# Optimization experiments

Measured on AMD Instinct MI355X. Metric: run time of the kernel, lower is better.

The kernel has to match this reference:

```python
import jax, jax.numpy as jnp
from jax import lax
import numpy as np

S, B, I, H = 1024, 512, 5, 32
G = 4 * H  # torch LSTM gate dim, order: i, f, g, o


def setup_inputs() -> dict:
    key = jax.random.key(0)
    ks = jax.random.split(key, 19)
    n = lambda k, shape, s=0.1: jax.random.normal(k, shape, jnp.float32) * s
    return {
        "x": jax.random.normal(ks[0], (S, B, I), jnp.float32),
        "Wih0": n(ks[1], (G, I)), "Whh0": n(ks[2], (G, H)), "bih0": n(ks[3], (G,)), "bhh0": n(ks[4], (G,)),
        "Wih1": n(ks[5], (G, H)), "Whh1": n(ks[6], (G, H)), "bih1": n(ks[7], (G,)), "bhh1": n(ks[8], (G,)),
        "Wih2": n(ks[9], (G, H)), "Whh2": n(ks[10], (G, H)), "bih2": n(ks[11], (G,)), "bhh2": n(ks[12], (G,)),
        "w1": n(ks[13], (H, H)), "b1": n(ks[14], (H,)),
        "w2": n(ks[15], (H, H)), "b2": n(ks[16], (H,)),
        "w3": n(ks[17], (1, H)), "b3": n(ks[18], (1,)),
    }


def lstm_layer(x, Wih, Whh, bih, bhh):
    # x: [S, B, in]; precompute input projections for all steps (one big GEMM)
    xp = jnp.einsum("sbi,gi->sbg", x, Wih) + bih + bhh  # [S, B, 4H]
    h0 = jnp.zeros((x.shape[1], H), x.dtype)
    c0 = jnp.zeros((x.shape[1], H), x.dtype)

    def step(carry, xg):
        h, c = carry
        gates = xg + h @ Whh.T  # [B, 4H]
        i, f, g, o = jnp.split(gates, 4, axis=-1)
        c = jax.nn.sigmoid(f) * c + jax.nn.sigmoid(i) * jnp.tanh(g)
        h = jax.nn.sigmoid(o) * jnp.tanh(c)
        return (h, c), h

    _, ys = lax.scan(step, (h0, c0), xp)
    return ys  # [S, B, H]


def reference(x, Wih0, Whh0, bih0, bhh0, Wih1, Whh1, bih1, bhh1,
              Wih2, Whh2, bih2, bhh2, w1, b1, w2, b2, w3, b3):
    h = lstm_layer(x, Wih0, Whh0, bih0, bhh0)
    h = lstm_layer(h, Wih1, Whh1, bih1, bhh1)
    h = lstm_layer(h, Wih2, Whh2, bih2, bhh2)  # [S, B, H]
    s, b, hd = h.shape
    y = h.reshape(s * b, hd)
    y = y @ w1.T + b1
    y = y @ w2.T + b2
    y = y @ w3.T + b3
    y = jax.nn.relu(y)
    return y.reshape(s, b, -1)  # [S, B, 1]
```

## Files before the change

kernel.cpp:

```cpp
#include <hip/hip_runtime.h>
#include <math.h>

#define S_LEN 1024
#define BATCH 512
#define HID   32

#define LOG2E 1.44269504088896340736f

__device__ __forceinline__ float fast_rcp(float x) { return __builtin_amdgcn_rcpf(x); }
__device__ __forceinline__ float fast_exp2(float x) { return __builtin_amdgcn_exp2f(x); }

__device__ __forceinline__ void tick_barrier() {
    asm volatile("s_waitcnt lgkmcnt(0)" ::: "memory");
    __builtin_amdgcn_s_barrier();
    asm volatile("" ::: "memory");
}

typedef unsigned int uint2v __attribute__((ext_vector_type(2)));
__device__ __forceinline__ void swap_halves(float v, float& hiAll, float& loAll) {
    uint2v r = __builtin_amdgcn_permlane32_swap(__float_as_uint(v),
                                                __float_as_uint(v),
                                                false, false);
    hiAll = __uint_as_float(r[0]);
    loAll = __uint_as_float(r[1]);
}

__device__ __forceinline__ float bcast(float v, int k) {
    return __int_as_float(__builtin_amdgcn_readlane(__float_as_int(v), k));
}

__device__ __forceinline__ float wave_sum64_dpp(float v) {
    float s = v;
    s += __int_as_float(__builtin_amdgcn_update_dpp(
             0, __float_as_int(s), 0x111, 0xf, 0xf, true));
    s += __int_as_float(__builtin_amdgcn_update_dpp(
             0, __float_as_int(s), 0x112, 0xf, 0xf, true));
    s += __int_as_float(__builtin_amdgcn_update_dpp(
             0, __float_as_int(s), 0x114, 0xf, 0xf, true));
    s += __int_as_float(__builtin_amdgcn_update_dpp(
             0, __float_as_int(s), 0x118, 0xf, 0xf, true));
    s += __int_as_float(__builtin_amdgcn_update_dpp(
             0, __float_as_int(s), 0x142, 0xa, 0xf, true));
    s += __int_as_float(__builtin_amdgcn_update_dpp(
             0, __float_as_int(s), 0x143, 0xc, 0xf, true));
    return s;
}

#define LOADROW(dst, base, row, sc)                                            \
    {                                                                          \
        const float4* W_ = reinterpret_cast<const float4*>((base) +            \
                                                    (size_t)(row) * HID);      \
        _Pragma("unroll")                                                      \
        for (int k4 = 0; k4 < 8; ++k4) {                                       \
            float4 v_ = W_[k4];                                                \
            dst[4 * k4 + 0] = v_.x * (sc);                                     \
            dst[4 * k4 + 1] = v_.y * (sc);                                     \
            dst[4 * k4 + 2] = v_.z * (sc);                                     \
            dst[4 * k4 + 3] = v_.w * (sc);                                     \
        }                                                                      \
    }

__global__ __launch_bounds__(192)
__attribute__((amdgpu_waves_per_eu(2)))
void lstm3_fused(const float* __restrict__ x,
                 const float* __restrict__ Wih0, const float* __restrict__ Whh0,
                 const float* __restrict__ bih0, const float* __restrict__ bhh0,
                 const float* __restrict__ Wih1, const float* __restrict__ Whh1,
                 const float* __restrict__ bih1, const float* __restrict__ bhh1,
                 const float* __restrict__ Wih2, const float* __restrict__ Whh2,
                 const float* __restrict__ bih2, const float* __restrict__ bhh2,
                 const float* __restrict__ w1, const float* __restrict__ b1,
                 const float* __restrict__ w2, const float* __restrict__ b2,
                 const float* __restrict__ w3, const float* __restrict__ b3,
                 float* __restrict__ out)
{
    const int b = blockIdx.x;
    const int w = threadIdx.x >> 6;
    const int l = threadIdx.x & 63;
    const int j = l & 31;
    const bool lowHalf = (l < 32);
    const int gA = l;
    const int gB = l + 64;
    const float sA = LOG2E;
    const float sB = lowHalf ? (2.0f * LOG2E) : LOG2E;

    __shared__ float4 xl4[S_LEN];
    __shared__ float  xl1[S_LEN];
    __shared__ float ring[4][2][HID];

    for (int i = threadIdx.x; i < 4 * 2 * HID; i += 192)
        (&ring[0][0][0])[i] = 0.0f;
    {
        float* xf = reinterpret_cast<float*>(xl4);
        for (int idx = threadIdx.x; idx < S_LEN * 5; idx += 192) {
            const int s = idx / 5;
            const int c = idx - 5 * s;
            const float v = x[(size_t)s * (BATCH * 5) + b * 5 + c];
            if (c < 4) xf[s * 4 + c] = v;
            else       xl1[s] = v;
        }
    }

    const float* Wih = (w == 0) ? Wih0 : (w == 1) ? Wih1 : Wih2;
    const float* Whh = (w == 0) ? Whh0 : (w == 1) ? Whh1 : Whh2;
    const float* bih = (w == 0) ? bih0 : (w == 1) ? bih1 : bih2;
    const float* bhh = (w == 0) ? bhh0 : (w == 1) ? bhh1 : bhh2;

    float whA[HID], whB[HID];
    LOADROW(whA, Whh, gA, sA);
    LOADROW(whB, Whh, gB, sB);
    float wiA[HID], wiB[HID];
    float wxA[5], wxB[5];
    if (w == 0) {
#pragma unroll
        for (int k = 0; k < 5; ++k) {
            wxA[k] = Wih[gA * 5 + k] * sA;
            wxB[k] = Wih[gB * 5 + k] * sB;
        }
    } else {
        LOADROW(wiA, Wih, gA, sA);
        LOADROW(wiB, Wih, gB, sB);
    }
    const float biasA = (bih[gA] + bhh[gA]) * sA;
    const float biasB = (bih[gB] + bhh[gB]) * sB;

    float v_j = 0.0f, cbias = 0.0f;
    if (w == 2) {
        float uacc[HID];
#pragma unroll
        for (int k = 0; k < HID; ++k) uacc[k] = 0.0f;
        for (int r = 0; r < HID; ++r) {
            const float w3r = w3[r];
#pragma unroll
            for (int k = 0; k < HID; ++k)
                uacc[k] += w3r * w2[r * HID + k];
        }
#pragma unroll
        for (int k = 0; k < HID; ++k) {
            v_j   += uacc[k] * w1[k * HID + j];
            cbias += uacc[k] * b1[k];
        }
        for (int r = 0; r < HID; ++r) cbias += w3[r] * b2[r];
        cbias += b3[0];
        v_j *= 0.5f;
    }

    float c = 0.0f;
    float h_own = 0.0f;

    __syncthreads();

#pragma unroll 1
    for (int t = 0; t < S_LEN + 4; ++t) {
        const int s = t - 2 * w;
        const bool active = (s >= 0) && (s < S_LEN);
        const int wslot = t & 3;
        const int rslot = wslot ^ 2;

        float aA0 = biasA, aA1 = 0.f, aA2 = 0.f, aA3 = 0.f;
        float aB0 = biasB, aB1 = 0.f, aB2 = 0.f, aB3 = 0.f;

#pragma unroll
        for (int k4 = 0; k4 < HID / 4; ++k4) {
            const float h0 = bcast(h_own, 4 * k4 + 0);
            const float h1 = bcast(h_own, 4 * k4 + 1);
            const float h2 = bcast(h_own, 4 * k4 + 2);
            const float h3 = bcast(h_own, 4 * k4 + 3);
            aA0 += whA[4 * k4 + 0] * h0;
            aA1 += whA[4 * k4 + 1] * h1;
            aA2 += whA[4 * k4 + 2] * h2;
            aA3 += whA[4 * k4 + 3] * h3;
            aB0 += whB[4 * k4 + 0] * h0;
            aB1 += whB[4 * k4 + 1] * h1;
            aB2 += whB[4 * k4 + 2] * h2;
            aB3 += whB[4 * k4 + 3] * h3;
        }

        if (w == 0) {
            if (active) {
                const float4 xv = xl4[s];
                const float  x4 = xl1[s];
                aA0 += wxA[0] * xv.x; aB0 += wxB[0] * xv.x;
                aA1 += wxA[1] * xv.y; aB1 += wxB[1] * xv.y;
                aA2 += wxA[2] * xv.z; aB2 += wxB[2] * xv.z;
                aA3 += wxA[3] * xv.w; aB3 += wxB[3] * xv.w;
                aA0 += wxA[4] * x4;   aB0 += wxB[4] * x4;
            }
        } else {
            const float4* hin4 =
                reinterpret_cast<const float4*>(&ring[rslot][w - 1][0]);
#pragma unroll
            for (int k4 = 0; k4 < HID / 4; ++k4) {
                float4 hv = hin4[k4];
                aA0 += wiA[4 * k4 + 0] * hv.x;
                aA1 += wiA[4 * k4 + 1] * hv.y;
                aA2 += wiA[4 * k4 + 2] * hv.z;
                aA3 += wiA[4 * k4 + 3] * hv.w;
                aB0 += wiB[4 * k4 + 0] * hv.x;
                aB1 += wiB[4 * k4 + 1] * hv.y;
                aB2 += wiB[4 * k4 + 2] * hv.z;
                aB3 += wiB[4 * k4 + 3] * hv.w;
            }
        }
        const float accA = (aA0 + aA1) + (aA2 + aA3);
        const float accB = (aB0 + aB1) + (aB2 + aB3);

        float yf, yi, yo, yg;
        swap_halves(accA, yf, yi);
        swap_halves(accB, yo, yg);

        const float gi = fast_rcp(1.0f + fast_exp2(-yi));
        const float gf = fast_rcp(1.0f + fast_exp2(-yf));
        const float sg = fast_rcp(1.0f + fast_exp2(-yg));
        const float go = fast_rcp(1.0f + fast_exp2(-yo));
        const float gg = 2.0f * sg - 1.0f;

        const float c_new = gf * c + gi * gg;
        const float e  = fast_exp2(-2.0f * LOG2E * fabsf(c_new));
        const float tc = copysignf((1.0f - e) * fast_rcp(1.0f + e), c_new);
        const float h = go * tc;

        if (active) {
            c = c_new;
            h_own = h;
            if (w < 2) {
                if (lowHalf) ring[wslot][w][j] = h;
            } else {
                const float tot = wave_sum64_dpp(h * v_j);
                const float y = fmaxf(tot + cbias, 0.0f);
                if (l == 63)
                    out[(size_t)s * BATCH + b] = y;
            }
        }
        if (t & 1) tick_barrier();
    }
}

extern "C" void kernel_launch(void* const* d_in, const int* in_sizes, int n_in,
                              void* d_out, int out_size, void* d_ws, size_t ws_size,
                              hipStream_t stream)
{
    const float* x    = (const float*)d_in[0];
    const float* Wih0 = (const float*)d_in[1];
    const float* Whh0 = (const float*)d_in[2];
    const float* bih0 = (const float*)d_in[3];
    const float* bhh0 = (const float*)d_in[4];
    const float* Wih1 = (const float*)d_in[5];
    const float* Whh1 = (const float*)d_in[6];
    const float* bih1 = (const float*)d_in[7];
    const float* bhh1 = (const float*)d_in[8];
    const float* Wih2 = (const float*)d_in[9];
    const float* Whh2 = (const float*)d_in[10];
    const float* bih2 = (const float*)d_in[11];
    const float* bhh2 = (const float*)d_in[12];
    const float* w1   = (const float*)d_in[13];
    const float* b1   = (const float*)d_in[14];
    const float* w2   = (const float*)d_in[15];
    const float* b2   = (const float*)d_in[16];
    const float* w3   = (const float*)d_in[17];
    const float* b3   = (const float*)d_in[18];

    lstm3_fused<<<BATCH, 192, 0, stream>>>(x, Wih0, Whh0, bih0, bhh0,
                                           Wih1, Whh1, bih1, bhh1,
                                           Wih2, Whh2, bih2, bhh2,
                                           w1, b1, w2, b2, w3, b3,
                                           (float*)d_out);
}
```

Baseline: 848.1 us.

## Run all three LSTM layers sequentially in one wave per batch element

Replaces the three-wave, layer-pipelined block (one wave per layer, communicating through an LDS ring with barriers) with a single 64-thread wave that computes all three layers each timestep. Whh0/Whh1 stay in registers, while Wih1, Wih2 and Whh2 are staged into LDS with an XOR swizzle to avoid bank conflicts. The layer-2 recurrent matvec is issued early to overlap with the layer-0 work. This removes the per-tick block barriers and the ring traffic. In exchange each wave's serial chain per step becomes roughly three times longer, and it relies on LDS reads plus more register pressure.

```diff
diff --git a/kernel.cpp b/kernel.cpp
--- a/kernel.cpp
+++ b/kernel.cpp
@@ -9,12 +9,6 @@
 
 __device__ __forceinline__ float fast_rcp(float x) { return __builtin_amdgcn_rcpf(x); }
 __device__ __forceinline__ float fast_exp2(float x) { return __builtin_amdgcn_exp2f(x); }
-
-__device__ __forceinline__ void tick_barrier() {
-    asm volatile("s_waitcnt lgkmcnt(0)" ::: "memory");
-    __builtin_amdgcn_s_barrier();
-    asm volatile("" ::: "memory");
-}
 
 typedef unsigned int uint2v __attribute__((ext_vector_type(2)));
 __device__ __forceinline__ void swap_halves(float v, float& hiAll, float& loAll) {
@@ -60,72 +54,62 @@
         }                                                                      \
     }
 
-__global__ __launch_bounds__(192)
-__attribute__((amdgpu_waves_per_eu(2)))
-void lstm3_fused(const float* __restrict__ x,
-                 const float* __restrict__ Wih0, const float* __restrict__ Whh0,
-                 const float* __restrict__ bih0, const float* __restrict__ bhh0,
-                 const float* __restrict__ Wih1, const float* __restrict__ Whh1,
-                 const float* __restrict__ bih1, const float* __restrict__ bhh1,
-                 const float* __restrict__ Wih2, const float* __restrict__ Whh2,
-                 const float* __restrict__ bih2, const float* __restrict__ bhh2,
-                 const float* __restrict__ w1, const float* __restrict__ b1,
-                 const float* __restrict__ w2, const float* __restrict__ b2,
-                 const float* __restrict__ w3, const float* __restrict__ b3,
-                 float* __restrict__ out)
+__global__ __launch_bounds__(64, 1)
+void lstm3_seq(const float* __restrict__ x,
+               const float* __restrict__ Wih0, const float* __restrict__ Whh0,
+               const float* __restrict__ bih0, const float* __restrict__ bhh0,
+               const float* __restrict__ Wih1, const float* __restrict__ Whh1,
+               const float* __restrict__ bih1, const float* __restrict__ bhh1,
+               const float* __restrict__ Wih2, const float* __restrict__ Whh2,
+               const float* __restrict__ bih2, const float* __restrict__ bhh2,
+               const float* __restrict__ w1, const float* __restrict__ b1,
+               const float* __restrict__ w2, const float* __restrict__ b2,
+               const float* __restrict__ w3, const float* __restrict__ b3,
+               float* __restrict__ out)
 {
     const int b = blockIdx.x;
-    const int w = threadIdx.x >> 6;
     const int l = threadIdx.x & 63;
     const int j = l & 31;
     const bool lowHalf = (l < 32);
     const int gA = l;
     const int gB = l + 64;
+    const int andA = l & 7;
     const float sA = LOG2E;
     const float sB = lowHalf ? (2.0f * LOG2E) : LOG2E;
 
-    __shared__ float4 xl4[S_LEN];
-    __shared__ float  xl1[S_LEN];
-    __shared__ float ring[4][2][HID];
-
-    for (int i = threadIdx.x; i < 4 * 2 * HID; i += 192)
-        (&ring[0][0][0])[i] = 0.0f;
+    __shared__ float wlds[3 * 128 * 32];
+
+    for (int i4 = l; i4 < 3 * 1024; i4 += 64) {
+        const int set = i4 >> 10;
+        const int rem = i4 & 1023;
+        const int row = rem >> 3;
+        const int k4  = rem & 7;
+        const float* W = (set == 0) ? Wih1 : (set == 1) ? Wih2 : Whh2;
+        float4 v = *reinterpret_cast<const float4*>(W + row * HID + k4 * 4);
+        const float sc = (row >= 64 && row < 96) ? 2.0f * LOG2E : LOG2E;
+        v.x *= sc; v.y *= sc; v.z *= sc; v.w *= sc;
+        *reinterpret_cast<float4*>(
+            &wlds[(set << 12) + row * HID + ((k4 ^ (row & 7)) << 2)]) = v;
+    }
+
+    float whA0[HID], whB0[HID], whA1[HID], whB1[HID];
+    LOADROW(whA0, Whh0, gA, sA); LOADROW(whB0, Whh0, gB, sB);
+    LOADROW(whA1, Whh1, gA, sA); LOADROW(whB1, Whh1, gB, sB);
+    float wxA[5], wxB[5];
+#pragma unroll
+    for (int k = 0; k < 5; ++k) {
+        wxA[k] = Wih0[gA * 5 + k] * sA;
+        wxB[k] = Wih0[gB * 5 + k] * sB;
+    }
+    const float b0A = (bih0[gA] + bhh0[gA]) * sA;
+    const float b0B = (bih0[gB] + bhh0[gB]) * sB;
+    const float b1A = (bih1[gA] + bhh1[gA]) * sA;
+    const float b1B = (bih1[gB] + bhh1[gB]) * sB;
+    const float b2A = (bih2[gA] + bhh2[gA]) * sA;
+    const float b2B = (bih2[gB] + bhh2[gB]) * sB;
+
+    float v_j = 0.0f, cbias = 0.0f;
     {
-        float* xf = reinterpret_cast<float*>(xl4);
-        for (int idx = threadIdx.x; idx < S_LEN * 5; idx += 192) {
-            const int s = idx / 5;
-            const int c = idx - 5 * s;
-            const float v = x[(size_t)s * (BATCH * 5) + b * 5 + c];
-            if (c < 4) xf[s * 4 + c] = v;
-            else       xl1[s] = v;
-        }
-    }
-
-    const float* Wih = (w == 0) ? Wih0 : (w == 1) ? Wih1 : Wih2;
-    const float* Whh = (w == 0) ? Whh0 : (w == 1) ? Whh1 : Whh2;
-    const float* bih = (w == 0) ? bih0 : (w == 1) ? bih1 : bih2;
-    const float* bhh = (w == 0) ? bhh0 : (w == 1) ? bhh1 : bhh2;
-
-    float whA[HID], whB[HID];
-    LOADROW(whA, Whh, gA, sA);
-    LOADROW(whB, Whh, gB, sB);
-    float wiA[HID], wiB[HID];
-    float wxA[5], wxB[5];
-    if (w == 0) {
-#pragma unroll
-        for (int k = 0; k < 5; ++k) {
-            wxA[k] = Wih[gA * 5 + k] * sA;
-            wxB[k] = Wih[gB * 5 + k] * sB;
-        }
-    } else {
-        LOADROW(wiA, Wih, gA, sA);
-        LOADROW(wiB, Wih, gB, sB);
-    }
-    const float biasA = (bih[gA] + bhh[gA]) * sA;
-    const float biasB = (bih[gB] + bhh[gB]) * sB;
-
-    float v_j = 0.0f, cbias = 0.0f;
-    if (w == 2) {
         float uacc[HID];
 #pragma unroll
         for (int k = 0; k < HID; ++k) uacc[k] = 0.0f;
@@ -145,95 +129,106 @@
         v_j *= 0.5f;
     }
 
-    float c = 0.0f;
-    float h_own = 0.0f;
-
-    __syncthreads();
+    float h0 = 0.f, h1 = 0.f, h2 = 0.f, c0 = 0.f, c1 = 0.f, c2 = 0.f;
+
+    const float* xb = x + (size_t)b * 5;
+    float xv0 = xb[0], xv1 = xb[1], xv2 = xb[2], xv3 = xb[3], xv4 = xb[4];
+
+#define MATVEC_LDS(setbase, hsrc, A0, A1, A2, A3, B0, B1, B2, B3)              \
+    _Pragma("unroll")                                                          \
+    for (int k4 = 0; k4 < 8; ++k4) {                                           \
+        const int perm = ((k4 ^ andA) << 2);                                   \
+        const float4 wa = *reinterpret_cast<const float4*>(                    \
+            &wlds[(setbase) + gA * HID + perm]);                               \
+        const float4 wb = *reinterpret_cast<const float4*>(                    \
+            &wlds[(setbase) + gB * HID + perm]);                               \
+        const float hh0 = bcast(hsrc, 4 * k4 + 0);                             \
+        const float hh1 = bcast(hsrc, 4 * k4 + 1);                             \
+        const float hh2 = bcast(hsrc, 4 * k4 + 2);                             \
+        const float hh3 = bcast(hsrc, 4 * k4 + 3);                             \
+        A0 += wa.x * hh0; A1 += wa.y * hh1;                                    \
+        A2 += wa.z * hh2; A3 += wa.w * hh3;                                    \
+        B0 += wb.x * hh0; B1 += wb.y * hh1;                                    \
+        B2 += wb.z * hh2; B3 += wb.w * hh3;                                    \
+    }
+
+#define MATVEC_REG(WA, WB, hsrc, A0, A1, A2, A3, B0, B1, B2, B3)               \
+    _Pragma("unroll")                                                          \
+    for (int k4 = 0; k4 < 8; ++k4) {                                           \
+        const float hh0 = bcast(hsrc, 4 * k4 + 0);                             \
+        const float hh1 = bcast(hsrc, 4 * k4 + 1);                             \
+        const float hh2 = bcast(hsrc, 4 * k4 + 2);                             \
+        const float hh3 = bcast(hsrc, 4 * k4 + 3);                             \
+        A0 += WA[4 * k4 + 0] * hh0; A1 += WA[4 * k4 + 1] * hh1;                \
+        A2 += WA[4 * k4 + 2] * hh2; A3 += WA[4 * k4 + 3] * hh3;                \
+        B0 += WB[4 * k4 + 0] * hh0; B1 += WB[4 * k4 + 1] * hh1;                \
+        B2 += WB[4 * k4 + 2] * hh2; B3 += WB[4 * k4 + 3] * hh3;                \
+    }
+
+#define TAIL(A0, A1, A2, A3, B0, B1, B2, B3, cvar, hvar)                       \
+    {                                                                          \
+        const float accA = ((A0) + (A1)) + ((A2) + (A3));                      \
+        const float accB = ((B0) + (B1)) + ((B2) + (B3));                      \
+        float yf, yi, yo, yg;                                                  \
+        swap_halves(accA, yf, yi);                                             \
+        swap_halves(accB, yo, yg);                                             \
+        const float gi = fast_rcp(1.0f + fast_exp2(-yi));                      \
+        const float gf = fast_rcp(1.0f + fast_exp2(-yf));                      \
+        const float sg = fast_rcp(1.0f + fast_exp2(-yg));                      \
+        const float go = fast_rcp(1.0f + fast_exp2(-yo));                      \
+        const float gg = 2.0f * sg - 1.0f;                                     \
+        const float cn = gf * (cvar) + gi * gg;                                \
+        const float e_ = fast_exp2(-2.0f * LOG2E * fabsf(cn));                 \
+        const float tc = copysignf((1.0f - e_) * fast_rcp(1.0f + e_), cn);     \
+        (cvar) = cn;                                                           \
+        (hvar) = go * tc;                                                      \
+    }
 
 #pragma unroll 1
-    for (int t = 0; t < S_LEN + 4; ++t) {
-        const int s = t - 2 * w;
-        const bool active = (s >= 0) && (s < S_LEN);
-        const int wslot = t & 3;
-        const int rslot = wslot ^ 2;
-
-        float aA0 = biasA, aA1 = 0.f, aA2 = 0.f, aA3 = 0.f;
-        float aB0 = biasB, aB1 = 0.f, aB2 = 0.f, aB3 = 0.f;
-
-#pragma unroll
-        for (int k4 = 0; k4 < HID / 4; ++k4) {
-            const float h0 = bcast(h_own, 4 * k4 + 0);
-            const float h1 = bcast(h_own, 4 * k4 + 1);
-            const float h2 = bcast(h_own, 4 * k4 + 2);
-            const float h3 = bcast(h_own, 4 * k4 + 3);
-            aA0 += whA[4 * k4 + 0] * h0;
-            aA1 += whA[4 * k4 + 1] * h1;
-            aA2 += whA[4 * k4 + 2] * h2;
-            aA3 += whA[4 * k4 + 3] * h3;
-            aB0 += whB[4 * k4 + 0] * h0;
-            aB1 += whB[4 * k4 + 1] * h1;
-            aB2 += whB[4 * k4 + 2] * h2;
-            aB3 += whB[4 * k4 + 3] * h3;
+    for (int t = 0; t < S_LEN; ++t) {
+        float a0A0 = b0A, a0A1 = 0.f, a0A2 = 0.f, a0A3 = 0.f;
+        float a0B0 = b0B, a0B1 = 0.f, a0B2 = 0.f, a0B3 = 0.f;
+        a0A0 += wxA[0] * xv0; a0B0 += wxB[0] * xv0;
+        a0A1 += wxA[1] * xv1; a0B1 += wxB[1] * xv1;
+        a0A2 += wxA[2] * xv2; a0B2 += wxB[2] * xv2;
+        a0A3 += wxA[3] * xv3; a0B3 += wxB[3] * xv3;
+        a0A0 += wxA[4] * xv4; a0B0 += wxB[4] * xv4;
+        MATVEC_REG(whA0, whB0, h0, a0A0, a0A1, a0A2, a0A3,
+                                   a0B0, a0B1, a0B2, a0B3);
+
+        float a1A0 = b1A, a1A1 = 0.f, a1A2 = 0.f, a1A3 = 0.f;
+        float a1B0 = b1B, a1B1 = 0.f, a1B2 = 0.f, a1B3 = 0.f;
+        MATVEC_REG(whA1, whB1, h1, a1A0, a1A1, a1A2, a1A3,
+                                   a1B0, a1B1, a1B2, a1B3);
+
+        float a2A0 = b2A, a2A1 = 0.f, a2A2 = 0.f, a2A3 = 0.f;
+        float a2B0 = b2B, a2B1 = 0.f, a2B2 = 0.f, a2B3 = 0.f;
+        MATVEC_LDS(2 << 12, h2, a2A0, a2A1, a2A2, a2A3,
+                                a2B0, a2B1, a2B2, a2B3);
+
+        if (t + 1 < S_LEN) {
+            const float* xn = xb + (size_t)(t + 1) * (BATCH * 5);
+            xv0 = xn[0]; xv1 = xn[1]; xv2 = xn[2]; xv3 = xn[3]; xv4 = xn[4];
         }
 
-        if (w == 0) {
-            if (active) {
-                const float4 xv = xl4[s];
-                const float  x4 = xl1[s];
-                aA0 += wxA[0] * xv.x; aB0 += wxB[0] * xv.x;
-                aA1 += wxA[1] * xv.y; aB1 += wxB[1] * xv.y;
-                aA2 += wxA[2] * xv.z; aB2 += wxB[2] * xv.z;
-                aA3 += wxA[3] * xv.w; aB3 += wxB[3] * xv.w;
-                aA0 += wxA[4] * x4;   aB0 += wxB[4] * x4;
-            }
-        } else {
-            const float4* hin4 =
-                reinterpret_cast<const float4*>(&ring[rslot][w - 1][0]);
-#pragma unroll
-            for (int k4 = 0; k4 < HID / 4; ++k4) {
-                float4 hv = hin4[k4];
-                aA0 += wiA[4 * k4 + 0] * hv.x;
-                aA1 += wiA[4 * k4 + 1] * hv.y;
-                aA2 += wiA[4 * k4 + 2] * hv.z;
-                aA3 += wiA[4 * k4 + 3] * hv.w;
-                aB0 += wiB[4 * k4 + 0] * hv.x;
-                aB1 += wiB[4 * k4 + 1] * hv.y;
-                aB2 += wiB[4 * k4 + 2] * hv.z;
-                aB3 += wiB[4 * k4 + 3] * hv.w;
-            }
-        }
-        const float accA = (aA0 + aA1) + (aA2 + aA3);
-        const float accB = (aB0 + aB1) + (aB2 + aB3);
-
-        float yf, yi, yo, yg;
-        swap_halves(accA, yf, yi);
-        swap_halves(accB, yo, yg);
-
-        const float gi = fast_rcp(1.0f + fast_exp2(-yi));
-        const float gf = fast_rcp(1.0f + fast_exp2(-yf));
-        const float sg = fast_rcp(1.0f + fast_exp2(-yg));
-        const float go = fast_rcp(1.0f + fast_exp2(-yo));
-        const float gg = 2.0f * sg - 1.0f;
-
-        const float c_new = gf * c + gi * gg;
-        const float e  = fast_exp2(-2.0f * LOG2E * fabsf(c_new));
-        const float tc = copysignf((1.0f - e) * fast_rcp(1.0f + e), c_new);
-        const float h = go * tc;
-
-        if (active) {
-            c = c_new;
-            h_own = h;
-            if (w < 2) {
-                if (lowHalf) ring[wslot][w][j] = h;
-            } else {
-                const float tot = wave_sum64_dpp(h * v_j);
-                const float y = fmaxf(tot + cbias, 0.0f);
-                if (l == 63)
-                    out[(size_t)s * BATCH + b] = y;
-            }
-        }
-        if (t & 1) tick_barrier();
-    }
+        TAIL(a0A0, a0A1, a0A2, a0A3, a0B0, a0B1, a0B2, a0B3, c0, h0);
+
+        MATVEC_LDS(0 << 12, h0, a1A0, a1A1, a1A2, a1A3,
+                                a1B0, a1B1, a1B2, a1B3);
+        TAIL(a1A0, a1A1, a1A2, a1A3, a1B0, a1B1, a1B2, a1B3, c1, h1);
+
+        MATVEC_LDS(1 << 12, h1, a2A0, a2A1, a2A2, a2A3,
+                                a2B0, a2B1, a2B2, a2B3);
+        TAIL(a2A0, a2A1, a2A2, a2A3, a2B0, a2B1, a2B2, a2B3, c2, h2);
+
+        const float tot = wave_sum64_dpp(h2 * v_j);
+        const float y = fmaxf(tot + cbias, 0.0f);
+        if (l == 63)
+            out[(size_t)t * BATCH + b] = y;
+    }
+#undef MATVEC_LDS
+#undef MATVEC_REG
+#undef TAIL
 }
 
 extern "C" void kernel_launch(void* const* d_in, const int* in_sizes, int n_in,
@@ -260,9 +255,9 @@
     const float* w3   = (const float*)d_in[17];
     const float* b3   = (const float*)d_in[18];
 
-    lstm3_fused<<<BATCH, 192, 0, stream>>>(x, Wih0, Whh0, bih0, bhh0,
-                                           Wih1, Whh1, bih1, bhh1,
-                                           Wih2, Whh2, bih2, bhh2,
-                                           w1, b1, w2, b2, w3, b3,
-                                           (float*)d_out);
-}
+    lstm3_seq<<<BATCH, 64, 0, stream>>>(x, Wih0, Whh0, bih0, bhh0,
+                                        Wih1, Whh1, bih1, bhh1,
+                                        Wih2, Whh2, bih2, bhh2,
+                                        w1, b1, w2, b2, w3, b3,
+                                        (float*)d_out);
+}
```

Measured after the change: 1.846 ms. +117.6%, slower.

## Unroll LSTM wavefront loop by four with one barrier per four ticks

Applied to the files above, without the earlier changes.

The time loop is unrolled by four ticks, and the ring buffer between layer waves grows from 4 to 8 slots. The inter-layer skew becomes 4 steps instead of 2, so only one workgroup barrier is needed per four ticks instead of one per two. The next tick's input projection is also interleaved with the previous tick's nonlinearity tail to hide latency. This adds register pressure and four extra ticks of pipeline fill. For wave 0 the input guard now checks only tt<S_LEN, relying on the later act_ check for correctness.

```diff
diff --git a/kernel.cpp b/kernel.cpp
--- a/kernel.cpp
+++ b/kernel.cpp
@@ -86,9 +86,9 @@
 
     __shared__ float4 xl4[S_LEN];
     __shared__ float  xl1[S_LEN];
-    __shared__ float ring[4][2][HID];
-
-    for (int i = threadIdx.x; i < 4 * 2 * HID; i += 192)
+    __shared__ float ring[8][2][HID];
+
+    for (int i = threadIdx.x; i < 8 * 2 * HID; i += 192)
         (&ring[0][0][0])[i] = 0.0f;
     {
         float* xf = reinterpret_cast<float*>(xl4);
@@ -150,90 +150,106 @@
 
     __syncthreads();
 
+#define TICK_INIT(n)                                                           \
+    float aA0_##n = biasA, aA1_##n = 0.f, aA2_##n = 0.f, aA3_##n = 0.f;        \
+    float aB0_##n = biasB, aB1_##n = 0.f, aB2_##n = 0.f, aB3_##n = 0.f;
+
+#define TICK_INPUT(n, tt)                                                      \
+    if (w == 0) {                                                              \
+        if ((tt) < S_LEN) {                                                    \
+            const float4 xv = xl4[(tt)];                                       \
+            const float  x4 = xl1[(tt)];                                       \
+            aA0_##n += wxA[0] * xv.x; aB0_##n += wxB[0] * xv.x;                \
+            aA1_##n += wxA[1] * xv.y; aB1_##n += wxB[1] * xv.y;                \
+            aA2_##n += wxA[2] * xv.z; aB2_##n += wxB[2] * xv.z;                \
+            aA3_##n += wxA[3] * xv.w; aB3_##n += wxB[3] * xv.w;                \
+            aA0_##n += wxA[4] * x4;   aB0_##n += wxB[4] * x4;                  \
+        }                                                                      \
+    } else {                                                                   \
+        const float4* hin4 =                                                   \
+            reinterpret_cast<const float4*>(&ring[((tt) & 7) ^ 4][w - 1][0]);  \
+        _Pragma("unroll")                                                      \
+        for (int k4 = 0; k4 < 8; ++k4) {                                       \
+            const float4 hv = hin4[k4];                                        \
+            aA0_##n += wiA[4 * k4 + 0] * hv.x;                                 \
+            aA1_##n += wiA[4 * k4 + 1] * hv.y;                                 \
+            aA2_##n += wiA[4 * k4 + 2] * hv.z;                                 \
+            aA3_##n += wiA[4 * k4 + 3] * hv.w;                                 \
+            aB0_##n += wiB[4 * k4 + 0] * hv.x;                                 \
+            aB1_##n += wiB[4 * k4 + 1] * hv.y;                                 \
+            aB2_##n += wiB[4 * k4 + 2] * hv.z;                                 \
+            aB3_##n += wiB[4 * k4 + 3] * hv.w;                                 \
+        }                                                                      \
+    }
+
+#define TICK_OWN(n)                                                            \
+    _Pragma("unroll")                                                          \
+    for (int k4 = 0; k4 < 8; ++k4) {                                           \
+        const float h0_ = bcast(h_own, 4 * k4 + 0);                            \
+        const float h1_ = bcast(h_own, 4 * k4 + 1);                            \
+        const float h2_ = bcast(h_own, 4 * k4 + 2);                            \
+        const float h3_ = bcast(h_own, 4 * k4 + 3);                            \
+        aA0_##n += whA[4 * k4 + 0] * h0_;                                      \
+        aA1_##n += whA[4 * k4 + 1] * h1_;                                      \
+        aA2_##n += whA[4 * k4 + 2] * h2_;                                      \
+        aA3_##n += whA[4 * k4 + 3] * h3_;                                      \
+        aB0_##n += whB[4 * k4 + 0] * h0_;                                      \
+        aB1_##n += whB[4 * k4 + 1] * h1_;                                      \
+        aB2_##n += whB[4 * k4 + 2] * h2_;                                      \
+        aB3_##n += whB[4 * k4 + 3] * h3_;                                      \
+    }
+
+#define TICK_TAIL(n, tt)                                                       \
+    {                                                                          \
+        const int s_ = (tt) - 4 * w;                                           \
+        const bool act_ = (s_ >= 0) && (s_ < S_LEN);                           \
+        const float accA = (aA0_##n + aA1_##n) + (aA2_##n + aA3_##n);          \
+        const float accB = (aB0_##n + aB1_##n) + (aB2_##n + aB3_##n);          \
+        float yf, yi, yo, yg;                                                  \
+        swap_halves(accA, yf, yi);                                             \
+        swap_halves(accB, yo, yg);                                             \
+        const float gi = fast_rcp(1.0f + fast_exp2(-yi));                      \
+        const float gf = fast_rcp(1.0f + fast_exp2(-yf));                      \
+        const float sg = fast_rcp(1.0f + fast_exp2(-yg));                      \
+        const float go = fast_rcp(1.0f + fast_exp2(-yo));                      \
+        const float gg = 2.0f * sg - 1.0f;                                     \
+        const float cn = gf * c + gi * gg;                                     \
+        const float e_ = fast_exp2(-2.0f * LOG2E * fabsf(cn));                 \
+        const float tc = copysignf((1.0f - e_) * fast_rcp(1.0f + e_), cn);     \
+        const float hh = go * tc;                                              \
+        if (act_) {                                                            \
+            c = cn;                                                            \
+            h_own = hh;                                                        \
+            if (w < 2) {                                                       \
+                if (lowHalf) ring[(tt) & 7][w][j] = hh;                        \
+            } else {                                                           \
+                const float tot = wave_sum64_dpp(hh * v_j);                    \
+                const float y = fmaxf(tot + cbias, 0.0f);                      \
+                if (l == 63) out[(size_t)s_ * BATCH + b] = y;                  \
+            }                                                                  \
+        }                                                                      \
+    }
+
 #pragma unroll 1
-    for (int t = 0; t < S_LEN + 4; ++t) {
-        const int s = t - 2 * w;
-        const bool active = (s >= 0) && (s < S_LEN);
-        const int wslot = t & 3;
-        const int rslot = wslot ^ 2;
-
-        float aA0 = biasA, aA1 = 0.f, aA2 = 0.f, aA3 = 0.f;
-        float aB0 = biasB, aB1 = 0.f, aB2 = 0.f, aB3 = 0.f;
-
-#pragma unroll
-        for (int k4 = 0; k4 < HID / 4; ++k4) {
-            const float h0 = bcast(h_own, 4 * k4 + 0);
-            const float h1 = bcast(h_own, 4 * k4 + 1);
-            const float h2 = bcast(h_own, 4 * k4 + 2);
-            const float h3 = bcast(h_own, 4 * k4 + 3);
-            aA0 += whA[4 * k4 + 0] * h0;
-            aA1 += whA[4 * k4 + 1] * h1;
-            aA2 += whA[4 * k4 + 2] * h2;
-            aA3 += whA[4 * k4 + 3] * h3;
-            aB0 += whB[4 * k4 + 0] * h0;
-            aB1 += whB[4 * k4 + 1] * h1;
-            aB2 += whB[4 * k4 + 2] * h2;
-            aB3 += whB[4 * k4 + 3] * h3;
-        }
-
-        if (w == 0) {
-            if (active) {
-                const float4 xv = xl4[s];
-                const float  x4 = xl1[s];
-                aA0 += wxA[0] * xv.x; aB0 += wxB[0] * xv.x;
-                aA1 += wxA[1] * xv.y; aB1 += wxB[1] * xv.y;
-                aA2 += wxA[2] * xv.z; aB2 += wxB[2] * xv.z;
-                aA3 += wxA[3] * xv.w; aB3 += wxB[3] * xv.w;
-                aA0 += wxA[4] * x4;   aB0 += wxB[4] * x4;
-            }
-        } else {
-            const float4* hin4 =
-                reinterpret_cast<const float4*>(&ring[rslot][w - 1][0]);
-#pragma unroll
-            for (int k4 = 0; k4 < HID / 4; ++k4) {
-                float4 hv = hin4[k4];
-                aA0 += wiA[4 * k4 + 0] * hv.x;
-                aA1 += wiA[4 * k4 + 1] * hv.y;
-                aA2 += wiA[4 * k4 + 2] * hv.z;
-                aA3 += wiA[4 * k4 + 3] * hv.w;
-                aB0 += wiB[4 * k4 + 0] * hv.x;
-                aB1 += wiB[4 * k4 + 1] * hv.y;
-                aB2 += wiB[4 * k4 + 2] * hv.z;
-                aB3 += wiB[4 * k4 + 3] * hv.w;
-            }
-        }
-        const float accA = (aA0 + aA1) + (aA2 + aA3);
-        const float accB = (aB0 + aB1) + (aB2 + aB3);
-
-        float yf, yi, yo, yg;
-        swap_halves(accA, yf, yi);
-        swap_halves(accB, yo, yg);
-
-        const float gi = fast_rcp(1.0f + fast_exp2(-yi));
-        const float gf = fast_rcp(1.0f + fast_exp2(-yf));
-        const float sg = fast_rcp(1.0f + fast_exp2(-yg));
-        const float go = fast_rcp(1.0f + fast_exp2(-yo));
-        const float gg = 2.0f * sg - 1.0f;
-
-        const float c_new = gf * c + gi * gg;
-        const float e  = fast_exp2(-2.0f * LOG2E * fabsf(c_new));
-        const float tc = copysignf((1.0f - e) * fast_rcp(1.0f + e), c_new);
-        const float h = go * tc;
-
-        if (active) {
-            c = c_new;
-            h_own = h;
-            if (w < 2) {
-                if (lowHalf) ring[wslot][w][j] = h;
-            } else {
-                const float tot = wave_sum64_dpp(h * v_j);
-                const float y = fmaxf(tot + cbias, 0.0f);
-                if (l == 63)
-                    out[(size_t)s * BATCH + b] = y;
-            }
-        }
-        if (t & 1) tick_barrier();
-    }
+    for (int t = 0; t < S_LEN + 8; t += 4) {
+        TICK_INIT(0) TICK_INPUT(0, t + 0)
+        TICK_OWN(0)
+        TICK_INIT(1) TICK_INPUT(1, t + 1)
+        TICK_TAIL(0, t + 0)
+        TICK_OWN(1)
+        TICK_INIT(2) TICK_INPUT(2, t + 2)
+        TICK_TAIL(1, t + 1)
+        TICK_OWN(2)
+        TICK_INIT(3) TICK_INPUT(3, t + 3)
+        TICK_TAIL(2, t + 2)
+        TICK_OWN(3)
+        TICK_TAIL(3, t + 3)
+        tick_barrier();
+    }
+#undef TICK_INIT
+#undef TICK_INPUT
+#undef TICK_OWN
+#undef TICK_TAIL
 }
 
 extern "C" void kernel_launch(void* const* d_in, const int* in_sizes, int n_in,
```

Result: slower. 1.012 ms (+19.3%).

## Replace workgroup barriers with LDS flag-based producer/consumer sync between layer waves

Applied to the files above, without the earlier changes.

Replaces the lockstep wavefront pipeline, which hit a workgroup barrier every two ticks, with per-wave progress counters in LDS. Each layer wave spins on its producer's counter and its consumer's read counter through an 8-slot ring buffer. This lets the three layer waves run decoupled instead of waiting on the slowest wave each tick. In exchange it adds spin-wait polling and relies on LDS write ordering within a wave without explicit waitcnt or fence, which may risk visibility races.

```diff
diff --git a/kernel.cpp b/kernel.cpp
--- a/kernel.cpp
+++ b/kernel.cpp
@@ -9,12 +9,6 @@
 
 __device__ __forceinline__ float fast_rcp(float x) { return __builtin_amdgcn_rcpf(x); }
 __device__ __forceinline__ float fast_exp2(float x) { return __builtin_amdgcn_exp2f(x); }
-
-__device__ __forceinline__ void tick_barrier() {
-    asm volatile("s_waitcnt lgkmcnt(0)" ::: "memory");
-    __builtin_amdgcn_s_barrier();
-    asm volatile("" ::: "memory");
-}
 
 typedef unsigned int uint2v __attribute__((ext_vector_type(2)));
 __device__ __forceinline__ void swap_halves(float v, float& hiAll, float& loAll) {
@@ -62,7 +56,7 @@
 
 __global__ __launch_bounds__(192)
 __attribute__((amdgpu_waves_per_eu(2)))
-void lstm3_fused(const float* __restrict__ x,
+void lstm3_async(const float* __restrict__ x,
                  const float* __restrict__ Wih0, const float* __restrict__ Whh0,
                  const float* __restrict__ bih0, const float* __restrict__ bhh0,
                  const float* __restrict__ Wih1, const float* __restrict__ Whh1,
@@ -78,18 +72,18 @@
     const int w = threadIdx.x >> 6;
     const int l = threadIdx.x & 63;
     const int j = l & 31;
-    const bool lowHalf = (l < 32);
     const int gA = l;
     const int gB = l + 64;
     const float sA = LOG2E;
-    const float sB = lowHalf ? (2.0f * LOG2E) : LOG2E;
+    const float sB = (l < 32) ? (2.0f * LOG2E) : LOG2E;
 
     __shared__ float4 xl4[S_LEN];
     __shared__ float  xl1[S_LEN];
-    __shared__ float ring[4][2][HID];
-
-    for (int i = threadIdx.x; i < 4 * 2 * HID; i += 192)
-        (&ring[0][0][0])[i] = 0.0f;
+    __shared__ float ring[8][2][HID];
+    __shared__ int syncv[8];
+    volatile int* const vs = (volatile int*)syncv;
+
+    if (threadIdx.x < 8) syncv[threadIdx.x] = 0;
     {
         float* xf = reinterpret_cast<float*>(xl4);
         for (int idx = threadIdx.x; idx < S_LEN * 5; idx += 192) {
@@ -150,12 +144,27 @@
 
     __syncthreads();
 
+    int Ppref = 0;
+    int Cpref = 0;
+
 #pragma unroll 1
-    for (int t = 0; t < S_LEN + 4; ++t) {
-        const int s = t - 2 * w;
-        const bool active = (s >= 0) && (s < S_LEN);
-        const int wslot = t & 3;
-        const int rslot = wslot ^ 2;
+    for (int s = 0; s < S_LEN; ++s) {
+        const int slot = s & 7;
+
+        if (w > 0 && Ppref < s + 1) {
+            int p;
+            do { p = vs[w - 1]; } while (p < s + 1);
+            Ppref = p;
+        }
+        if (w < 2 && Cpref < s - 7) {
+            int q;
+            do { q = vs[4 + w]; } while (q < s - 7);
+            Cpref = q;
+        }
+        asm volatile("" ::: "memory");
+
+        if (w > 0) Ppref = vs[w - 1];
+        if (w < 2) Cpref = vs[4 + w];
 
         float aA0 = biasA, aA1 = 0.f, aA2 = 0.f, aA3 = 0.f;
         float aB0 = biasB, aB1 = 0.f, aB2 = 0.f, aB3 = 0.f;
@@ -177,21 +186,19 @@
         }
 
         if (w == 0) {
-            if (active) {
-                const float4 xv = xl4[s];
-                const float  x4 = xl1[s];
-                aA0 += wxA[0] * xv.x; aB0 += wxB[0] * xv.x;
-                aA1 += wxA[1] * xv.y; aB1 += wxB[1] * xv.y;
-                aA2 += wxA[2] * xv.z; aB2 += wxB[2] * xv.z;
-                aA3 += wxA[3] * xv.w; aB3 += wxB[3] * xv.w;
-                aA0 += wxA[4] * x4;   aB0 += wxB[4] * x4;
-            }
+            const float4 xv = xl4[s];
+            const float  x4 = xl1[s];
+            aA0 += wxA[0] * xv.x; aB0 += wxB[0] * xv.x;
+            aA1 += wxA[1] * xv.y; aB1 += wxB[1] * xv.y;
+            aA2 += wxA[2] * xv.z; aB2 += wxB[2] * xv.z;
+            aA3 += wxA[3] * xv.w; aB3 += wxB[3] * xv.w;
+            aA0 += wxA[4] * x4;   aB0 += wxB[4] * x4;
         } else {
             const float4* hin4 =
-                reinterpret_cast<const float4*>(&ring[rslot][w - 1][0]);
+                reinterpret_cast<const float4*>(&ring[slot][w - 1][0]);
 #pragma unroll
             for (int k4 = 0; k4 < HID / 4; ++k4) {
-                float4 hv = hin4[k4];
+                const float4 hv = hin4[k4];
                 aA0 += wiA[4 * k4 + 0] * hv.x;
                 aA1 += wiA[4 * k4 + 1] * hv.y;
                 aA2 += wiA[4 * k4 + 2] * hv.z;
@@ -201,6 +208,8 @@
                 aB2 += wiB[4 * k4 + 2] * hv.z;
                 aB3 += wiB[4 * k4 + 3] * hv.w;
             }
+            asm volatile("" ::: "memory");
+            if (l == 0) vs[4 + (w - 1)] = s + 1;
         }
         const float accA = (aA0 + aA1) + (aA2 + aA3);
         const float accB = (aB0 + aB1) + (aB2 + aB3);
@@ -220,19 +229,18 @@
         const float tc = copysignf((1.0f - e) * fast_rcp(1.0f + e), c_new);
         const float h = go * tc;
 
-        if (active) {
-            c = c_new;
-            h_own = h;
-            if (w < 2) {
-                if (lowHalf) ring[wslot][w][j] = h;
-            } else {
-                const float tot = wave_sum64_dpp(h * v_j);
-                const float y = fmaxf(tot + cbias, 0.0f);
-                if (l == 63)
-                    out[(size_t)s * BATCH + b] = y;
-            }
-        }
-        if (t & 1) tick_barrier();
+        c = c_new;
+        h_own = h;
+        if (w < 2) {
+            if (l < 32) ring[slot][w][j] = h;
+            asm volatile("" ::: "memory");
+            if (l == 0) vs[w] = s + 1;
+        } else {
+            const float tot = wave_sum64_dpp(h * v_j);
+            const float y = fmaxf(tot + cbias, 0.0f);
+            if (l == 63)
+                out[(size_t)s * BATCH + b] = y;
+        }
     }
 }
 
@@ -260,7 +268,7 @@
     const float* w3   = (const float*)d_in[17];
     const float* b3   = (const float*)d_in[18];
 
-    lstm3_fused<<<BATCH, 192, 0, stream>>>(x, Wih0, Whh0, bih0, bhh0,
+    lstm3_async<<<BATCH, 192, 0, stream>>>(x, Wih0, Whh0, bih0, bhh0,
                                            Wih1, Whh1, bih1, bhh1,
                                            Wih2, Whh2, bih2, bhh2,
                                            w1, b1, w2, b2, w3, b3,
```

Measured after the change: 951.6 us. 1.12x slower.
